# Optimization experiments

Measured on AMD Instinct MI355X. Metric: run time of the kernel, lower is better.

Reference implementation:

```python
import jax, jax.numpy as jnp
import numpy as np
import math

B, T, C, H = 2, 2048, 1024, 16
HD = C // H  # head dim = 64

def setup_inputs() -> dict:
    key = jax.random.key(0)
    ks = jax.random.split(key, 12)
    s = 0.02
    return {
        "x": jax.random.normal(ks[0], (B, T, C), dtype=jnp.float32),
        "ln1_g": jnp.ones((C,), jnp.float32),
        "ln1_b": jnp.zeros((C,), jnp.float32),
        "W_attn": jax.random.normal(ks[1], (C, 3 * C), jnp.float32) * s,
        "b_attn": jnp.zeros((3 * C,), jnp.float32),
        "W_ap": jax.random.normal(ks[2], (C, C), jnp.float32) * s,
        "b_ap": jnp.zeros((C,), jnp.float32),
        "ln2_g": jnp.ones((C,), jnp.float32),
        "ln2_b": jnp.zeros((C,), jnp.float32),
        "W_fc": jax.random.normal(ks[3], (C, 4 * C), jnp.float32) * s,
        "b_fc": jnp.zeros((4 * C,), jnp.float32),
        "W_mp": jax.random.normal(ks[4], (4 * C, C), jnp.float32) * s,
        "b_mp": jnp.zeros((C,), jnp.float32),
    }

def layernorm(x, g, b, eps=1e-5):
    mu = jnp.mean(x, axis=-1, keepdims=True)
    var = jnp.mean(jnp.square(x - mu), axis=-1, keepdims=True)
    return (x - mu) * jax.lax.rsqrt(var + eps) * g + b

def gelu_tanh(x):
    # GELU(approximate='tanh')
    c = math.sqrt(2.0 / math.pi)
    return 0.5 * x * (1.0 + jnp.tanh(c * (x + 0.044715 * x * x * x)))

def attention(x, W_attn, b_attn, W_ap, b_ap):
    b, t, c = x.shape
    qkv = x @ W_attn + b_attn                      # [B,T,3C]
    q, k, v = jnp.split(qkv, 3, axis=-1)
    q = q.reshape(b, t, H, HD).transpose(0, 2, 1, 3)  # [B,H,T,hd]
    k = k.reshape(b, t, H, HD).transpose(0, 2, 1, 3)
    v = v.reshape(b, t, H, HD).transpose(0, 2, 1, 3)
    attn = jnp.einsum('bhqd,bhkd->bhqk', q, k) * (1.0 / math.sqrt(HD))
    mask = jnp.tril(jnp.ones((t, t), dtype=bool))
    attn = jnp.where(mask, attn, jnp.float32(-jnp.inf))
    attn = jax.nn.softmax(attn, axis=-1)
    y = jnp.einsum('bhqk,bhkd->bhqd', attn, v)
    y = y.transpose(0, 2, 1, 3).reshape(b, t, c)
    return y @ W_ap + b_ap

def reference(x, ln1_g, ln1_b, W_attn, b_attn, W_ap, b_ap,
              ln2_g, ln2_b, W_fc, b_fc, W_mp, b_mp):
    x = x + attention(layernorm(x, ln1_g, ln1_b), W_attn, b_attn, W_ap, b_ap)
    h = layernorm(x, ln2_g, ln2_b)
    h = gelu_tanh(h @ W_fc + b_fc) @ W_mp + b_mp
    return x + h
```

## Files before the change

kernel.cpp:

```cpp
#include <hip/hip_runtime.h>
#include <stdint.h>

#define TT_ 2048
#define CC_ 1024

typedef unsigned short u16;
typedef __bf16 bf16x8 __attribute__((ext_vector_type(8)));
typedef __bf16 bf16x4 __attribute__((ext_vector_type(4)));
typedef float f32x4 __attribute__((ext_vector_type(4)));
typedef unsigned short u16x8 __attribute__((ext_vector_type(8)));

__device__ __forceinline__ u16 f2bf(float f) {
  unsigned u = __float_as_uint(f);
  u += 0x7fff + ((u >> 16) & 1);
  return (u16)(u >> 16);
}
__device__ __forceinline__ float bf2f(u16 v) {
  return __uint_as_float(((unsigned)v) << 16);
}

__device__ __forceinline__ float gelu_f(float t) {
  float u = 1.5957691216057308f * (t + 0.044715f * t * t * t);
  return t / (1.f + __expf(-u));
}

__device__ __forceinline__ void async_cp16(const u16* g, u16* l) {
  __builtin_amdgcn_global_load_lds(
      (const __attribute__((address_space(1))) void*)(uintptr_t)g,
      (__attribute__((address_space(3))) void*)(uint32_t)(uintptr_t)l,
      16, 0, 0);
}

__device__ __forceinline__ void blockbar() {
  asm volatile("" ::: "memory");
  __builtin_amdgcn_s_barrier();
  asm volatile("" ::: "memory");
}

__global__ __launch_bounds__(256) void kconv_t(const float* __restrict__ W,
                                               u16* __restrict__ WT, int K, int N) {
  __shared__ float t[32][33];
  int n0 = blockIdx.x * 32, k0 = blockIdx.y * 32;
  int tx = threadIdx.x & 31, ty = threadIdx.x >> 5;
#pragma unroll
  for (int r = 0; r < 4; ++r)
    t[ty + 8 * r][tx] = W[(size_t)(k0 + ty + 8 * r) * N + n0 + tx];
  __syncthreads();
#pragma unroll
  for (int r = 0; r < 4; ++r)
    WT[(size_t)(n0 + ty + 8 * r) * K + k0 + tx] = f2bf(t[tx][ty + 8 * r]);
}

__global__ __launch_bounds__(256) void kln(const float* __restrict__ x,
                                           const float* __restrict__ g,
                                           const float* __restrict__ b,
                                           u16* __restrict__ out) {
  int row = blockIdx.x, tid = threadIdx.x;
  const float4* xr = (const float4*)(x + (size_t)row * CC_);
  float4 v = xr[tid];
  float s = v.x + v.y + v.z + v.w;
  float s2 = v.x * v.x + v.y * v.y + v.z * v.z + v.w * v.w;
#pragma unroll
  for (int off = 32; off; off >>= 1) { s += __shfl_down(s, off); s2 += __shfl_down(s2, off); }
  __shared__ float rs[4], rq[4];
  int w = tid >> 6;
  if ((tid & 63) == 0) { rs[w] = s; rq[w] = s2; }
  __syncthreads();
  s = rs[0] + rs[1] + rs[2] + rs[3];
  s2 = rq[0] + rq[1] + rq[2] + rq[3];
  float mean = s * (1.f / CC_);
  float var = s2 * (1.f / CC_) - mean * mean;
  float rstd = rsqrtf(var + 1e-5f);
  float4 gv = ((const float4*)g)[tid];
  float4 bv = ((const float4*)b)[tid];
  u16* orow = out + (size_t)row * CC_ + tid * 4;
  orow[0] = f2bf((v.x - mean) * rstd * gv.x + bv.x);
  orow[1] = f2bf((v.y - mean) * rstd * gv.y + bv.y);
  orow[2] = f2bf((v.z - mean) * rstd * gv.z + bv.z);
  orow[3] = f2bf((v.w - mean) * rstd * gv.w + bv.w);
}

__global__ __launch_bounds__(256) void kln2(float* __restrict__ x1,
                                            const u16* __restrict__ part,
                                            const float* __restrict__ g,
                                            const float* __restrict__ b,
                                            u16* __restrict__ out) {
  int row = blockIdx.x, tid = threadIdx.x;
  float4* xr = (float4*)(x1 + (size_t)row * CC_);
  float4 v = xr[tid];
  bf16x4 pv = *(const bf16x4*)(part + (size_t)row * CC_ + tid * 4);
  v.x += (float)pv[0]; v.y += (float)pv[1]; v.z += (float)pv[2]; v.w += (float)pv[3];
  xr[tid] = v;
  float s = v.x + v.y + v.z + v.w;
  float s2 = v.x * v.x + v.y * v.y + v.z * v.z + v.w * v.w;
#pragma unroll
  for (int off = 32; off; off >>= 1) { s += __shfl_down(s, off); s2 += __shfl_down(s2, off); }
  __shared__ float rs[4], rq[4];
  int w = tid >> 6;
  if ((tid & 63) == 0) { rs[w] = s; rq[w] = s2; }
  __syncthreads();
  s = rs[0] + rs[1] + rs[2] + rs[3];
  s2 = rq[0] + rq[1] + rq[2] + rq[3];
  float mean = s * (1.f / CC_);
  float var = s2 * (1.f / CC_) - mean * mean;
  float rstd = rsqrtf(var + 1e-5f);
  float4 gv = ((const float4*)g)[tid];
  float4 bv = ((const float4*)b)[tid];
  u16* orow = out + (size_t)row * CC_ + tid * 4;
  orow[0] = f2bf((v.x - mean) * rstd * gv.x + bv.x);
  orow[1] = f2bf((v.y - mean) * rstd * gv.y + bv.y);
  orow[2] = f2bf((v.z - mean) * rstd * gv.z + bv.z);
  orow[3] = f2bf((v.w - mean) * rstd * gv.w + bv.w);
}

template <int EPI, int NSPLIT>
__global__ __launch_bounds__(256) void kgemm(const u16* __restrict__ A,
                                             const u16* __restrict__ BTm,
                                             const float* __restrict__ bias,
                                             const float* __restrict__ resid,
                                             void* __restrict__ out,
                                             u16* __restrict__ part,
                                             int M, int N, int Ktot,
                                             int chunks_x, int ychunks, int cx) {
  __shared__ __align__(16) u16 As[2][128 * 32];
  __shared__ __align__(16) u16 Bs[2][128 * 32];
  const int tid = threadIdx.x, lane = tid & 63, w = tid >> 6;
  const int llo = lane & 15, lhi = lane >> 4;

  const int bid = blockIdx.x;
  const int xcd = bid & 7, s = bid >> 3;
  const int chx = xcd % chunks_x, chyz = xcd / chunks_x;
  const int z = chyz / ychunks, chy = chyz % ychunks;
  const int bx = chx * cx + s % cx;
  const int cy = (gridDim.x >> 3) / cx;
  const int by = chy * cy + s / cx;

  const int row0 = by * 128, col0 = bx * 128;
  const int wr = w >> 1, wc = w & 1;
  const int crow = lane >> 2;
  const int ck = (lane & 3) * 8;
  const int Kc = Ktot / NSPLIT;
  const int klo = (NSPLIT > 1) ? z * Kc : 0;

  f32x4 acc[4][4] = {};

  auto stage = [&](int bufi, int kof) {
#pragma unroll
    for (int c = w; c < 8; c += 4) {
      int r = c * 16 + crow;
      async_cp16(A + (size_t)(row0 + r) * Ktot + klo + kof + ck, &As[bufi][c * 512]);
      async_cp16(BTm + (size_t)(col0 + r) * Ktot + klo + kof + ck, &Bs[bufi][c * 512]);
    }
  };

  const int nt = Kc / 32;
  stage(0, 0);
  asm volatile("s_waitcnt vmcnt(0)" ::: "memory");
  blockbar();
  int cur = 0;

  for (int t = 0; t < nt; ++t) {
    if (t + 1 < nt) stage(cur ^ 1, (t + 1) * 32);
    bf16x8 af[4], bfr[4];
#pragma unroll
    for (int m = 0; m < 4; ++m)
      af[m] = *(const bf16x8*)&As[cur][(wr * 64 + m * 16 + llo) * 32 + lhi * 8];
#pragma unroll
    for (int n = 0; n < 4; ++n)
      bfr[n] = *(const bf16x8*)&Bs[cur][(wc * 64 + n * 16 + llo) * 32 + lhi * 8];
#pragma unroll
    for (int m = 0; m < 4; ++m)
#pragma unroll
      for (int n = 0; n < 4; ++n)
        acc[m][n] = __builtin_amdgcn_mfma_f32_16x16x32_bf16(af[m], bfr[n], acc[m][n], 0, 0, 0);
    if (t + 1 < nt) {
      asm volatile("s_waitcnt vmcnt(0)" ::: "memory");
      blockbar();
    }
    cur ^= 1;
  }

  const int c_row = row0 + wr * 64 + lhi * 4;
  const int c_col = col0 + wc * 64 + llo;
  const bool fin = (NSPLIT == 1) || (z == 0);
  u16* pb = part + (NSPLIT > 1 ? ((size_t)(z > 0 ? z - 1 : 0)) * M * N : 0);

  if constexpr (EPI == 3) {
    if (col0 >= 2048) {
      const int b_ = c_row >> 11;
      const int tokb = c_row & 2047;
#pragma unroll
      for (int n = 0; n < 4; ++n) {
        int col = c_col + n * 16;
        float bb = bias[col];
        u16* vrow = part + (size_t)(b_ * 1024 + (col - 2048)) * TT_ + tokb;
#pragma unroll
        for (int m = 0; m < 4; ++m) {
          f32x4 a = acc[m][n];
          bf16x4 pk = {(__bf16)(a[0] + bb), (__bf16)(a[1] + bb),
                       (__bf16)(a[2] + bb), (__bf16)(a[3] + bb)};
          *(bf16x4*)(vrow + m * 16) = pk;
        }
      }
      return;
    }
  }

#pragma unroll
  for (int n = 0; n < 4; ++n) {
    int col = c_col + n * 16;
    float bb = bias[col];
#pragma unroll
    for (int m = 0; m < 4; ++m) {
      f32x4 a = acc[m][n];
#pragma unroll
      for (int i = 0; i < 4; ++i) {
        size_t idx = (size_t)(c_row + m * 16 + i) * N + col;
        if (!fin) {
          pb[idx] = f2bf(a[i]);
        } else {
          float val = a[i] + bb;
          if constexpr (EPI == 1) {
            ((float*)out)[idx] = val + resid[idx];
          } else if constexpr (EPI == 2) {
            ((u16*)out)[idx] = f2bf(gelu_f(val));
          } else {
            ((u16*)out)[idx] = f2bf(val);
          }
        }
      }
    }
  }
}

__global__ __launch_bounds__(256) void kadd1(float* __restrict__ out,
                                             const u16* __restrict__ p) {
  size_t i0 = ((size_t)blockIdx.x * 256 + threadIdx.x) * 8;
  float4 o0 = *(float4*)(out + i0);
  float4 o1 = *(float4*)(out + i0 + 4);
  u16x8 v = *(const u16x8*)(p + i0);
  o0.x += bf2f(v[0]); o0.y += bf2f(v[1]); o0.z += bf2f(v[2]); o0.w += bf2f(v[3]);
  o1.x += bf2f(v[4]); o1.y += bf2f(v[5]); o1.z += bf2f(v[6]); o1.w += bf2f(v[7]);
  *(float4*)(out + i0) = o0;
  *(float4*)(out + i0 + 4) = o1;
}

__global__ __launch_bounds__(256, 4) void kattn(const u16* __restrict__ qkv,
                                                const u16* __restrict__ VT,
                                                u16* __restrict__ y) {
  const int h = blockIdx.x, b = blockIdx.y, z = blockIdx.z;
  const int tid = threadIdx.x, lane = tid & 63, w = tid >> 6;
  const int llo = lane & 15, lhi = lane >> 4;

  __shared__ __align__(16) u16 Qs[64 * 64];
  __shared__ __align__(16) u16 Ks[2][64 * 64];
  __shared__ __align__(16) u16 Vs[2][64 * 64];
  __shared__ __align__(16) u16 Ps[64 * 72];

  const size_t tok0 = (size_t)b * TT_;
  const u16* qb = qkv + tok0 * 3072 + h * 64;
  const u16* kb = qb + 1024;

  const u16 *kg[2], *vg[2];
#pragma unroll
  for (int it = 0; it < 2; ++it) {
    int p_ = w * 16 + it * 8 + (lane >> 3);
    int krow = ((p_ & 15) << 2) | (p_ >> 4);
    int scol = ((lane & 7) * 8) ^ ((p_ & 7) << 3);
    kg[it] = kb + (size_t)krow * 3072 + scol;
    vg[it] = VT + ((size_t)(b * 16 + h) * 64 + p_) * TT_ + scol;
  }

  auto stageKV = [&](int bufi, int j) {
    async_cp16(kg[0] + (size_t)j * (64 * 3072), &Ks[bufi][(w * 16 + 0) * 64]);
    async_cp16(kg[1] + (size_t)j * (64 * 3072), &Ks[bufi][(w * 16 + 8) * 64]);
    async_cp16(vg[0] + (size_t)j * 64, &Vs[bufi][(w * 16 + 0) * 64]);
    async_cp16(vg[1] + (size_t)j * 64, &Vs[bufi][(w * 16 + 8) * 64]);
  };

  const float alpha = 0.18033688011112042f;
  const int r8 = tid >> 3, ce = (tid & 7) * 8;

#pragma unroll 1
  for (int ph = 0; ph < 2; ++ph) {
    const int qt = ph ? (31 - z) : z;
    const int q0 = qt * 64;

#pragma unroll
    for (int it = 0; it < 2; ++it) {
      int tk = it * 32 + r8;
      u16x8 v = *(const u16x8*)(qb + (size_t)(q0 + tk) * 3072 + ce);
#pragma unroll
      for (int e = 0; e < 8; ++e) v[e] = f2bf(bf2f(v[e]) * alpha);
      *(u16x8*)&Qs[tk * 64 + (ce ^ ((tk & 7) << 3))] = v;
    }
    asm volatile("s_waitcnt lgkmcnt(0)" ::: "memory");
    stageKV(0, 0);
    blockbar();

    bf16x8 aq[2];
#pragma unroll
    for (int kk = 0; kk < 2; ++kk)
      aq[kk] = *(const bf16x8*)&Qs[(w * 16 + llo) * 64 +
                                   ((kk * 32 + lhi * 8) ^ ((llo & 7) << 3))];

    float l_i[4] = {0.f, 0.f, 0.f, 0.f};
    f32x4 o[4] = {};

    int buf = 0;
    for (int j = 0; j <= qt; ++j) {
      if (j < qt) {
        stageKV(buf ^ 1, j + 1);
        asm volatile("s_waitcnt vmcnt(4)" ::: "memory");
      } else {
        asm volatile("s_waitcnt vmcnt(0)" ::: "memory");
      }
      blockbar();

      f32x4 s[4] = {};
      __builtin_amdgcn_s_setprio(1);
#pragma unroll
      for (int nb = 0; nb < 4; ++nb)
#pragma unroll
        for (int kk = 0; kk < 2; ++kk) {
          bf16x8 bk = *(const bf16x8*)&Ks[buf][(nb * 16 + llo) * 64 +
                                              ((kk * 32 + lhi * 8) ^ ((llo & 7) << 3))];
          s[nb] = __builtin_amdgcn_mfma_f32_16x16x32_bf16(aq[kk], bk, s[nb], 0, 0, 0);
        }
      __builtin_amdgcn_s_setprio(0);

      if (j == qt) {
#pragma unroll
        for (int nb = 0; nb < 4; ++nb)
#pragma unroll
          for (int i = 0; i < 4; ++i)
            if (llo * 4 + nb > w * 16 + lhi * 4 + i) s[nb][i] = -1e30f;
      }

#pragma unroll
      for (int i = 0; i < 4; ++i) {
        float p0 = exp2f(s[0][i] - 8.f);
        float p1 = exp2f(s[1][i] - 8.f);
        float p2 = exp2f(s[2][i] - 8.f);
        float p3 = exp2f(s[3][i] - 8.f);
        l_i[i] += (p0 + p1) + (p2 + p3);
        bf16x4 pk = {(__bf16)p0, (__bf16)p1, (__bf16)p2, (__bf16)p3};
        *(bf16x4*)&Ps[(w * 16 + lhi * 4 + i) * 72 + llo * 4] = pk;
      }

      bf16x8 pa[2];
#pragma unroll
      for (int kk = 0; kk < 2; ++kk)
        pa[kk] = *(const bf16x8*)&Ps[(w * 16 + llo) * 72 + kk * 32 + lhi * 8];
      __builtin_amdgcn_s_setprio(1);
#pragma unroll
      for (int db = 0; db < 4; ++db)
#pragma unroll
        for (int kk = 0; kk < 2; ++kk) {
          bf16x8 bv = *(const bf16x8*)&Vs[buf][(db * 16 + llo) * 64 +
                                              ((kk * 32 + lhi * 8) ^ ((llo & 7) << 3))];
          o[db] = __builtin_amdgcn_mfma_f32_16x16x32_bf16(pa[kk], bv, o[db], 0, 0, 0);
        }
      __builtin_amdgcn_s_setprio(0);
      blockbar();
      buf ^= 1;
    }

#pragma unroll
    for (int i = 0; i < 4; ++i) {
      float t = l_i[i];
#pragma unroll
      for (int off = 1; off < 16; off <<= 1) t += __shfl_xor(t, off);
      float inv = 1.f / t;
      size_t row = tok0 + q0 + w * 16 + lhi * 4 + i;
#pragma unroll
      for (int db = 0; db < 4; ++db)
        y[row * CC_ + h * 64 + db * 16 + llo] = f2bf(o[db][i] * inv);
    }
  }
}

extern "C" void kernel_launch(void* const* d_in, const int* in_sizes, int n_in,
                              void* d_out, int out_size, void* d_ws, size_t ws_size,
                              hipStream_t stream) {
  (void)in_sizes; (void)n_in; (void)out_size; (void)ws_size;
  const float* x      = (const float*)d_in[0];
  const float* ln1g   = (const float*)d_in[1];
  const float* ln1b   = (const float*)d_in[2];
  const float* W_attn = (const float*)d_in[3];
  const float* b_attn = (const float*)d_in[4];
  const float* W_ap   = (const float*)d_in[5];
  const float* b_ap   = (const float*)d_in[6];
  const float* ln2g   = (const float*)d_in[7];
  const float* ln2b   = (const float*)d_in[8];
  const float* W_fc   = (const float*)d_in[9];
  const float* b_fc   = (const float*)d_in[10];
  const float* W_mp   = (const float*)d_in[11];
  const float* b_mp   = (const float*)d_in[12];

  char* p = (char*)d_ws;
  u16* WTmp   = (u16*)p; p += (size_t)4096 * 1024 * 2;
  u16* WTattn = (u16*)p; p += (size_t)3072 * 1024 * 2;
  u16* WTap   = (u16*)p; p += (size_t)1024 * 1024 * 2;
  u16* WTfc   = (u16*)p; p += (size_t)4096 * 1024 * 2;
  u16* xn     = (u16*)p; p += (size_t)4096 * 1024 * 2;
  u16* qkvb   = (u16*)p; p += (size_t)4096 * 3072 * 2;
  u16* yb     = (u16*)p; p += (size_t)4096 * 1024 * 2;
  float* x1   = (float*)p; p += (size_t)4096 * 1024 * 4;
  u16* h2     = (u16*)p; p += (size_t)4096 * 1024 * 2;
  u16* fcb    = qkvb;
  u16* VT     = (u16*)x1;
  u16* appart = xn;
  u16* mpp    = WTattn;

  kconv_t<<<dim3(96, 32), 256, 0, stream>>>(W_attn, WTattn, 1024, 3072);
  kconv_t<<<dim3(32, 32), 256, 0, stream>>>(W_ap, WTap, 1024, 1024);
  kconv_t<<<dim3(128, 32), 256, 0, stream>>>(W_fc, WTfc, 1024, 4096);
  kconv_t<<<dim3(32, 128), 256, 0, stream>>>(W_mp, WTmp, 4096, 1024);

  kln<<<4096, 256, 0, stream>>>(x, ln1g, ln1b, xn);
  kgemm<3, 1><<<768, 256, 0, stream>>>(xn, WTattn, b_attn, nullptr, qkvb, VT,
                                       4096, 3072, 1024, 2, 4, 12);
  kattn<<<dim3(16, 2, 16), 256, 0, stream>>>(qkvb, VT, yb);
  kgemm<1, 2><<<512, 256, 0, stream>>>(yb, WTap, b_ap, x, x1, appart,
                                       4096, 1024, 1024, 1, 4, 8);
  kln2<<<4096, 256, 0, stream>>>(x1, appart, ln2g, ln2b, h2);
  kgemm<2, 1><<<1024, 256, 0, stream>>>(h2, WTfc, b_fc, nullptr, fcb, nullptr,
                                        4096, 4096, 1024, 2, 4, 16);
  kgemm<1, 2><<<512, 256, 0, stream>>>(fcb, WTmp, b_mp, x1, (float*)d_out, mpp,
                                       4096, 1024, 4096, 1, 4, 8);
  kadd1<<<2048, 256, 0, stream>>>((float*)d_out, mpp);
}
```

Before: 262.8 us.

## Enlarge attention query tile to 128 rows and merge weight conversion launches

The attention kernel now processes 128 query rows per block with 8 waves, so each staged K/V tile is shared by twice as many waves, and waves skip tiles lying entirely above the causal diagonal. The grid is halved and occupancy is set to one 512-thread block per SM, which trades latency hiding for less K/V traffic. The four weight transpose/convert launches are folded into one kernel that dispatches on block index, cutting launch overhead.

```diff
diff --git a/kernel.cpp b/kernel.cpp
--- a/kernel.cpp
+++ b/kernel.cpp
@@ -37,10 +37,24 @@
   asm volatile("" ::: "memory");
 }
 
-__global__ __launch_bounds__(256) void kconv_t(const float* __restrict__ W,
-                                               u16* __restrict__ WT, int K, int N) {
+__global__ __launch_bounds__(256) void kconvall(const float* __restrict__ Wattn,
+                                                const float* __restrict__ Wap,
+                                                const float* __restrict__ Wfc,
+                                                const float* __restrict__ Wmp,
+                                                u16* __restrict__ WTattn,
+                                                u16* __restrict__ WTap,
+                                                u16* __restrict__ WTfc,
+                                                u16* __restrict__ WTmp) {
+  int bid = blockIdx.x;
+  const float* W; u16* WT; int K, N, lb;
+  if (bid < 3072)      { W = Wattn; WT = WTattn; K = 1024; N = 3072; lb = bid; }
+  else if (bid < 4096) { W = Wap;   WT = WTap;   K = 1024; N = 1024; lb = bid - 3072; }
+  else if (bid < 8192) { W = Wfc;   WT = WTfc;   K = 1024; N = 4096; lb = bid - 4096; }
+  else                 { W = Wmp;   WT = WTmp;   K = 4096; N = 1024; lb = bid - 8192; }
+  int nb = N >> 5;
+  int n0 = (lb % nb) * 32, k0 = (lb / nb) * 32;
+
   __shared__ float t[32][33];
-  int n0 = blockIdx.x * 32, k0 = blockIdx.y * 32;
   int tx = threadIdx.x & 31, ty = threadIdx.x >> 5;
 #pragma unroll
   for (int r = 0; r < 4; ++r)
@@ -245,37 +259,31 @@
   *(float4*)(out + i0 + 4) = o1;
 }
 
-__global__ __launch_bounds__(256, 4) void kattn(const u16* __restrict__ qkv,
+__global__ __launch_bounds__(512, 1) void kattn(const u16* __restrict__ qkv,
                                                 const u16* __restrict__ VT,
                                                 u16* __restrict__ y) {
   const int h = blockIdx.x, b = blockIdx.y, z = blockIdx.z;
   const int tid = threadIdx.x, lane = tid & 63, w = tid >> 6;
   const int llo = lane & 15, lhi = lane >> 4;
 
-  __shared__ __align__(16) u16 Qs[64 * 64];
+  __shared__ __align__(16) u16 Qs[128 * 64];
   __shared__ __align__(16) u16 Ks[2][64 * 64];
   __shared__ __align__(16) u16 Vs[2][64 * 64];
-  __shared__ __align__(16) u16 Ps[64 * 72];
+  __shared__ __align__(16) u16 Ps[128 * 72];
 
   const size_t tok0 = (size_t)b * TT_;
   const u16* qb = qkv + tok0 * 3072 + h * 64;
   const u16* kb = qb + 1024;
 
-  const u16 *kg[2], *vg[2];
-#pragma unroll
-  for (int it = 0; it < 2; ++it) {
-    int p_ = w * 16 + it * 8 + (lane >> 3);
-    int krow = ((p_ & 15) << 2) | (p_ >> 4);
-    int scol = ((lane & 7) * 8) ^ ((p_ & 7) << 3);
-    kg[it] = kb + (size_t)krow * 3072 + scol;
-    vg[it] = VT + ((size_t)(b * 16 + h) * 64 + p_) * TT_ + scol;
-  }
+  const int p_ = w * 8 + (lane >> 3);
+  const int krow = ((p_ & 15) << 2) | (p_ >> 4);
+  const int scol = ((lane & 7) * 8) ^ ((p_ & 7) << 3);
+  const u16* kg = kb + (size_t)krow * 3072 + scol;
+  const u16* vg = VT + ((size_t)(b * 16 + h) * 64 + p_) * TT_ + scol;
 
   auto stageKV = [&](int bufi, int j) {
-    async_cp16(kg[0] + (size_t)j * (64 * 3072), &Ks[bufi][(w * 16 + 0) * 64]);
-    async_cp16(kg[1] + (size_t)j * (64 * 3072), &Ks[bufi][(w * 16 + 8) * 64]);
-    async_cp16(vg[0] + (size_t)j * 64, &Vs[bufi][(w * 16 + 0) * 64]);
-    async_cp16(vg[1] + (size_t)j * 64, &Vs[bufi][(w * 16 + 8) * 64]);
+    async_cp16(kg + (size_t)j * (64 * 3072), &Ks[bufi][w * 512]);
+    async_cp16(vg + (size_t)j * 64, &Vs[bufi][w * 512]);
   };
 
   const float alpha = 0.18033688011112042f;
@@ -283,12 +291,13 @@
 
 #pragma unroll 1
   for (int ph = 0; ph < 2; ++ph) {
-    const int qt = ph ? (31 - z) : z;
-    const int q0 = qt * 64;
+    const int qt = ph ? (15 - z) : z;
+    const int q0 = qt * 128;
+    const int ntiles = 2 * qt + 2;
 
 #pragma unroll
     for (int it = 0; it < 2; ++it) {
-      int tk = it * 32 + r8;
+      int tk = it * 64 + r8;
       u16x8 v = *(const u16x8*)(qb + (size_t)(q0 + tk) * 3072 + ce);
 #pragma unroll
       for (int e = 0; e < 8; ++e) v[e] = f2bf(bf2f(v[e]) * alpha);
@@ -306,62 +315,66 @@
 
     float l_i[4] = {0.f, 0.f, 0.f, 0.f};
     f32x4 o[4] = {};
+    const int row_min = q0 + w * 16, row_max = row_min + 15;
 
     int buf = 0;
-    for (int j = 0; j <= qt; ++j) {
-      if (j < qt) {
+    for (int j = 0; j < ntiles; ++j) {
+      if (j + 1 < ntiles) {
         stageKV(buf ^ 1, j + 1);
-        asm volatile("s_waitcnt vmcnt(4)" ::: "memory");
+        asm volatile("s_waitcnt vmcnt(2)" ::: "memory");
       } else {
         asm volatile("s_waitcnt vmcnt(0)" ::: "memory");
       }
       blockbar();
 
-      f32x4 s[4] = {};
-      __builtin_amdgcn_s_setprio(1);
-#pragma unroll
-      for (int nb = 0; nb < 4; ++nb)
-#pragma unroll
-        for (int kk = 0; kk < 2; ++kk) {
-          bf16x8 bk = *(const bf16x8*)&Ks[buf][(nb * 16 + llo) * 64 +
-                                              ((kk * 32 + lhi * 8) ^ ((llo & 7) << 3))];
-          s[nb] = __builtin_amdgcn_mfma_f32_16x16x32_bf16(aq[kk], bk, s[nb], 0, 0, 0);
+      const int kmin = j * 64;
+      if (kmin <= row_max) {
+        f32x4 s[4] = {};
+        __builtin_amdgcn_s_setprio(1);
+#pragma unroll
+        for (int nb = 0; nb < 4; ++nb)
+#pragma unroll
+          for (int kk = 0; kk < 2; ++kk) {
+            bf16x8 bk = *(const bf16x8*)&Ks[buf][(nb * 16 + llo) * 64 +
+                                                ((kk * 32 + lhi * 8) ^ ((llo & 7) << 3))];
+            s[nb] = __builtin_amdgcn_mfma_f32_16x16x32_bf16(aq[kk], bk, s[nb], 0, 0, 0);
+          }
+        __builtin_amdgcn_s_setprio(0);
+
+        if (kmin + 63 > row_min) {
+#pragma unroll
+          for (int nb = 0; nb < 4; ++nb)
+#pragma unroll
+            for (int i = 0; i < 4; ++i)
+              if (kmin + llo * 4 + nb > row_min + lhi * 4 + i) s[nb][i] = -1e30f;
         }
-      __builtin_amdgcn_s_setprio(0);
-
-      if (j == qt) {
-#pragma unroll
-        for (int nb = 0; nb < 4; ++nb)
-#pragma unroll
-          for (int i = 0; i < 4; ++i)
-            if (llo * 4 + nb > w * 16 + lhi * 4 + i) s[nb][i] = -1e30f;
+
+#pragma unroll
+        for (int i = 0; i < 4; ++i) {
+          float p0 = exp2f(s[0][i] - 8.f);
+          float p1 = exp2f(s[1][i] - 8.f);
+          float p2 = exp2f(s[2][i] - 8.f);
+          float p3 = exp2f(s[3][i] - 8.f);
+          l_i[i] += (p0 + p1) + (p2 + p3);
+          bf16x4 pk = {(__bf16)p0, (__bf16)p1, (__bf16)p2, (__bf16)p3};
+          *(bf16x4*)&Ps[(w * 16 + lhi * 4 + i) * 72 + llo * 4] = pk;
+        }
+
+        bf16x8 pa[2];
+#pragma unroll
+        for (int kk = 0; kk < 2; ++kk)
+          pa[kk] = *(const bf16x8*)&Ps[(w * 16 + llo) * 72 + kk * 32 + lhi * 8];
+        __builtin_amdgcn_s_setprio(1);
+#pragma unroll
+        for (int db = 0; db < 4; ++db)
+#pragma unroll
+          for (int kk = 0; kk < 2; ++kk) {
+            bf16x8 bv = *(const bf16x8*)&Vs[buf][(db * 16 + llo) * 64 +
+                                                ((kk * 32 + lhi * 8) ^ ((llo & 7) << 3))];
+            o[db] = __builtin_amdgcn_mfma_f32_16x16x32_bf16(pa[kk], bv, o[db], 0, 0, 0);
+          }
+        __builtin_amdgcn_s_setprio(0);
       }
-
-#pragma unroll
-      for (int i = 0; i < 4; ++i) {
-        float p0 = exp2f(s[0][i] - 8.f);
-        float p1 = exp2f(s[1][i] - 8.f);
-        float p2 = exp2f(s[2][i] - 8.f);
-        float p3 = exp2f(s[3][i] - 8.f);
-        l_i[i] += (p0 + p1) + (p2 + p3);
-        bf16x4 pk = {(__bf16)p0, (__bf16)p1, (__bf16)p2, (__bf16)p3};
-        *(bf16x4*)&Ps[(w * 16 + lhi * 4 + i) * 72 + llo * 4] = pk;
-      }
-
-      bf16x8 pa[2];
-#pragma unroll
-      for (int kk = 0; kk < 2; ++kk)
-        pa[kk] = *(const bf16x8*)&Ps[(w * 16 + llo) * 72 + kk * 32 + lhi * 8];
-      __builtin_amdgcn_s_setprio(1);
-#pragma unroll
-      for (int db = 0; db < 4; ++db)
-#pragma unroll
-        for (int kk = 0; kk < 2; ++kk) {
-          bf16x8 bv = *(const bf16x8*)&Vs[buf][(db * 16 + llo) * 64 +
-                                              ((kk * 32 + lhi * 8) ^ ((llo & 7) << 3))];
-          o[db] = __builtin_amdgcn_mfma_f32_16x16x32_bf16(pa[kk], bv, o[db], 0, 0, 0);
-        }
-      __builtin_amdgcn_s_setprio(0);
       blockbar();
       buf ^= 1;
     }
@@ -413,15 +426,13 @@
   u16* appart = xn;
   u16* mpp    = WTattn;
 
-  kconv_t<<<dim3(96, 32), 256, 0, stream>>>(W_attn, WTattn, 1024, 3072);
-  kconv_t<<<dim3(32, 32), 256, 0, stream>>>(W_ap, WTap, 1024, 1024);
-  kconv_t<<<dim3(128, 32), 256, 0, stream>>>(W_fc, WTfc, 1024, 4096);
-  kconv_t<<<dim3(32, 128), 256, 0, stream>>>(W_mp, WTmp, 4096, 1024);
+  kconvall<<<12288, 256, 0, stream>>>(W_attn, W_ap, W_fc, W_mp,
+                                      WTattn, WTap, WTfc, WTmp);
 
   kln<<<4096, 256, 0, stream>>>(x, ln1g, ln1b, xn);
   kgemm<3, 1><<<768, 256, 0, stream>>>(xn, WTattn, b_attn, nullptr, qkvb, VT,
                                        4096, 3072, 1024, 2, 4, 12);
-  kattn<<<dim3(16, 2, 16), 256, 0, stream>>>(qkvb, VT, yb);
+  kattn<<<dim3(16, 2, 8), 512, 0, stream>>>(qkvb, VT, yb);
   kgemm<1, 2><<<512, 256, 0, stream>>>(yb, WTap, b_ap, x, x1, appart,
                                        4096, 1024, 1024, 1, 4, 8);
   kln2<<<4096, 256, 0, stream>>>(x1, appart, ln2g, ln2b, h2);
```

Result: faster. 254.4 us (-3.2%).
